# Optimization experiments

Hardware: AMD Instinct MI355X
Metric: run time of the kernel (lower is better)

The kernel has to match this reference:

```python
import jax, jax.numpy as jnp
import numpy as np

B, T, N, CIN = 64, 24, 256, 1  # batch, n_his, n stations, in channels
F1, F2, OUTC = 64, 128, 1      # blocks [[64,64],[64,128]], output channels
K = 3                          # conv kernel size


def conv2d_same(x, w):  # x [B,H,W,C], w [K,K,C,O]
    return jax.lax.conv_general_dilated(x, w, (1, 1), 'SAME',
                                        dimension_numbers=('NHWC', 'HWIO', 'NHWC'))


def conv1d_same(x, w):  # x [B,N,C], w [K,C,O]
    return jax.lax.conv_general_dilated(x, w, (1,), 'SAME',
                                        dimension_numbers=('NWC', 'WIO', 'NWC'))


def hard_sigmoid(x):  # keras ConvLSTM default recurrent_activation
    return jnp.clip(x * 0.2 + 0.5, 0.0, 1.0)


def l2_normalize_23(x):  # tf.nn.l2_normalize over axes [2,3]
    sq = jnp.sum(x * x, axis=(2, 3), keepdims=True)
    return x * jax.lax.rsqrt(jnp.maximum(sq, 1e-12))


def convlstm1d(x_seq, kx, kh, b, return_sequences):
    # x_seq [B,T,N,C]; kx [K,C,4F]; kh [K,F,4F]; b [4F]
    Bs, Ts, Ns, Cs = x_seq.shape
    F = kh.shape[1]
    # input convolutions are time-independent: do them all at once
    xg = conv1d_same(x_seq.reshape(Bs * Ts, Ns, Cs), kx).reshape(Bs, Ts, Ns, 4 * F) + b
    xg = jnp.moveaxis(xg, 1, 0)  # [T,B,N,4F]
    h0 = jnp.zeros((Bs, Ns, F), x_seq.dtype)
    c0 = jnp.zeros((Bs, Ns, F), x_seq.dtype)

    def step(carry, xt):
        h, c = carry
        g = xt + conv1d_same(h, kh)                 # [B,N,4F]
        gi, gf, gc, go = jnp.split(g, 4, axis=-1)
        i = hard_sigmoid(gi)
        f = hard_sigmoid(gf)
        o = hard_sigmoid(go)
        c = f * c + i * jnp.tanh(gc)
        h = o * jnp.tanh(c)
        return (h, c), (h if return_sequences else jnp.zeros((), x_seq.dtype))

    (hT, _), hs = jax.lax.scan(step, (h0, c0), xg)
    if return_sequences:
        return jnp.moveaxis(hs, 0, 1)  # [B,T,N,F]
    return hT                          # [B,N,F]


def setup_inputs() -> dict:
    key = jax.random.key(0)
    ks = jax.random.split(key, 14)
    s = 0.1
    return {
        'x': jax.random.normal(ks[0], (B, T, N, CIN), jnp.float32),
        'conv1_w': jax.random.normal(ks[1], (K, K, CIN, F1), jnp.float32) * s,
        'conv1_b': jnp.zeros((F1,), jnp.float32),
        'conv2_w': jax.random.normal(ks[2], (K, K, F1, F1), jnp.float32) * s,
        'conv2_b': jnp.zeros((F1,), jnp.float32),
        'kx1': jax.random.normal(ks[3], (K, F1, 4 * F1), jnp.float32) * s,
        'kh1': jax.random.normal(ks[4], (K, F1, 4 * F1), jnp.float32) * s,
        'b1': jnp.zeros((4 * F1,), jnp.float32),
        'kx2': jax.random.normal(ks[5], (K, F1, 4 * F2), jnp.float32) * s,
        'kh2': jax.random.normal(ks[6], (K, F2, 4 * F2), jnp.float32) * s,
        'b2': jnp.zeros((4 * F2,), jnp.float32),
        'fc_w': jax.random.normal(ks[7], (F2, OUTC), jnp.float32) * s,
        'fc_b': jnp.zeros((OUTC,), jnp.float32),
    }


def reference(x, conv1_w, conv1_b, conv2_w, conv2_b, kx1, kh1, b1,
              kx2, kh2, b2, fc_w, fc_b):
    # spatial conv stack (Conv2D 3x3 same, linear activation)
    h = conv2d_same(x, conv1_w) + conv1_b
    h = conv2d_same(h, conv2_w) + conv2_b
    # dropout = identity at inference; norm == 'L2'
    h = l2_normalize_23(h)
    # stacked ConvLSTM1D: return_sequences=True then False
    h = convlstm1d(h, kx1, kh1, b1, True)    # [B,T,N,F1]
    h = convlstm1d(h, kx2, kh2, b2, False)   # [B,N,F2]
    h = h[:, None]                            # reshape (-1, 1, N, F2)
    h = l2_normalize_23(h)
    # FullyConLayer: 1x1 FC over channels -> outc
    y = jnp.einsum('bunc,co->buno', h, fc_w) + fc_b
    return y.reshape(-1, 1, N, OUTC)
```

## Files before the change

kernel.cpp:

```cpp
#include <hip/hip_runtime.h>
#include <hip/hip_bf16.h>

using bf16 = __hip_bfloat16;
typedef unsigned short u16;
typedef unsigned int u32;
typedef __attribute__((ext_vector_type(8))) short short8;
typedef __attribute__((ext_vector_type(4))) float floatx4;

#define DEVI __device__ __forceinline__

constexpr int B = 64, T = 24, N = 256, F1 = 64, F2 = 128;

DEVI float b2f(bf16 v) { return __bfloat162float(v); }
DEVI float b2fu(u16 u) { return __uint_as_float(((u32)u) << 16); }
DEVI u16 f2b(float f) {
    u32 u = __float_as_uint(f);
    u32 r = (u + 0x7FFF + ((u >> 16) & 1)) >> 16;
    return (u16)r;
}
DEVI float hsig(float x) { x = x * 0.2f + 0.5f; return fminf(fmaxf(x, 0.f), 1.f); }

#if __has_builtin(__builtin_amdgcn_global_load_lds)
#define ASYNC16(gsrc, ldst)                                                            \
    __builtin_amdgcn_global_load_lds((const __attribute__((address_space(1))) u32*)(gsrc), \
                                     (__attribute__((address_space(3))) u32*)(ldst), 16, 0, 0)
#define HAVE_ASYNC 1
#else
#define HAVE_ASYNC 0
#endif

DEVI float read_in(const void* p, long i, int isbf) {
    return isbf ? b2f(((const bf16*)p)[i]) : ((const float*)p)[i];
}

__global__ void init_flag(int* flag) { *flag = 1; }
__global__ void detect_scan(const u16* __restrict__ xu, int* __restrict__ flag) {
    int i0 = blockIdx.x * 2048 + threadIdx.x;
    int hit = 0;
    for (int i = i0; i < (blockIdx.x + 1) * 2048; i += 256)
        if (((xu[i] >> 7) & 0xFF) == 0xFF) hit = 1;
    if (hit) *flag = 0;
}

struct CvtDesc { const void* src; float* dst; int n; };
struct CvtPack { CvtDesc d[8]; };
__global__ void cvt_pack(CvtPack p, const int* __restrict__ flag) {
    CvtDesc c = p.d[blockIdx.x];
    int isbf = *flag;
    for (int i = threadIdx.x; i < c.n; i += 256)
        c.dst[i] = c.src ? read_in(c.src, i, isbf) : 0.f;
}

__global__ void repack_w(const void* __restrict__ kxr, const void* __restrict__ khr,
                         u16* __restrict__ Wt, int CIN, int F, const int* __restrict__ flag) {
    int NG = 4 * F, CH = CIN + F, K = 3 * CH;
    int idx = blockIdx.x * 256 + threadIdx.x;
    if (idx >= NG * K) return;
    int g = idx / K, k = idx - g * K;
    int kn = k / CH, c = k - kn * CH;
    int isbf = *flag;
    float v = (c < CIN) ? read_in(kxr, (long)(kn * CIN + c) * NG + g, isbf)
                        : read_in(khr, (long)(kn * F + (c - CIN)) * NG + g, isbf);
    Wt[(long)g * K + k] = f2b(v);
}

__global__ void repack_w2(const void* __restrict__ w2r, u16* __restrict__ w2b,
                          const int* __restrict__ flag) {
    int idx = blockIdx.x * 256 + threadIdx.x;
    if (idx >= 64 * 576) return;
    int f = idx / 576, k = idx - f * 576;
    int kt = k / 192, rem = k - kt * 192, kn = rem >> 6, c = rem & 63;
    float v = read_in(w2r, (long)((kt * 3 + kn) * 64 + c) * 64 + f, *flag);
    w2b[(long)f * 576 + k] = f2b(v);
}

__global__ __launch_bounds__(256)
void conv1_all(const void* __restrict__ xraw, const float* __restrict__ w1c,
               const float* __restrict__ b1v, u16* __restrict__ c1all,
               const int* __restrict__ flag) {
    __shared__ float sxw[3 * 260];
    int s = blockIdx.x, b = blockIdx.y, tid = threadIdx.x;
    int tt = s - 1;
    u16* dst = c1all + ((long)s * B + b) * N * 64;
    if (tt < 0 || tt >= T) {
        for (int i = tid; i < N * 64 / 4; i += 256) *(uint2*)&dst[i * 4] = uint2{0, 0};
        return;
    }
    int isbf = *flag;
    for (int i = tid; i < 3 * 258; i += 256) {
        int r = i / 258, cc = i - r * 258;
        int ttt = tt - 1 + r, nn = cc - 1;
        float v = 0.f;
        if (ttt >= 0 && ttt < T && nn >= 0 && nn < N)
            v = read_in(xraw, (long)(b * T + ttt) * N + nn, isbf);
        sxw[r * 260 + cc] = v;
    }
    __syncthreads();
    int c = tid & 63, ngq = tid >> 6;
    float w[9];
#pragma unroll
    for (int j = 0; j < 9; j++) w[j] = w1c[j * 64 + c];
    float bias = b1v[c];
    for (int j = 0; j < 64; j++) {
        int n = ngq * 64 + j;
        float v = bias;
#pragma unroll
        for (int dt = 0; dt < 3; dt++)
#pragma unroll
            for (int dn = 0; dn < 3; dn++)
                v += sxw[dt * 260 + n + dn] * w[dt * 3 + dn];
        dst[n * 64 + c] = f2b(v);
    }
}

__global__ __launch_bounds__(256)
void conv_mfma(const u16* __restrict__ c1all, const u16* __restrict__ w2b,
               const float* __restrict__ b2v, u16* __restrict__ xs24,
               float* __restrict__ ssq) {
    constexpr int CP1 = 72;
    __shared__ __align__(16) u16 win1[3 * 66 * CP1];
    __shared__ __align__(16) u16 bch[2 * 2048];
    __shared__ float red[256];

    int tid = threadIdx.x;
    int bb = blockIdx.y, n0 = blockIdx.x * 64, t = blockIdx.z;
    int w = tid >> 6, l15 = tid & 15, q = (tid >> 4) & 3;

    for (int i = tid; i < 3 * 66 * 8; i += 256) {
        int u = i & 7, rr = i >> 3;
        int kt = rr / 66, r1 = rr - kt * 66;
        int nn = n0 - 1 + r1;
        uint4 v{0, 0, 0, 0};
        if (nn >= 0 && nn < N)
            v = *(const uint4*)&c1all[((((long)(t + kt)) * B + bb) * N + nn) * 64 + u * 8];
        *(uint4*)&win1[(kt * 66 + r1) * CP1 + u * 8] = v;
    }

    auto stage = [&](int kk, int bufi) {
        int g = tid >> 2, u = tid & 3;
        int k = kk * 32 + ((u ^ (g & 3)) << 3);
#if HAVE_ASYNC
        ASYNC16(w2b + (long)g * 576 + k, &bch[bufi * 2048 + tid * 8]);
#else
        uint4 v = *(const uint4*)(w2b + (long)g * 576 + k);
        *(uint4*)&bch[bufi * 2048 + tid * 8] = v;
#endif
    };
    stage(0, 0);
    __syncthreads();

    floatx4 acc[4] = {};
    for (int kk = 0; kk < 18; ++kk) {
        int cur = kk & 1;
        if (kk + 1 < 18) stage(kk + 1, 1 - cur);
        int kbase = kk * 32;
        int kt = kbase / 192, rem = kbase - kt * 192, kn = rem >> 6, c0 = rem & 63;
        int gcol = w * 16 + l15;
        short8 bf = *(const short8*)&bch[cur * 2048 + gcol * 32 + ((q ^ (gcol & 3)) << 3)];
#pragma unroll
        for (int mi = 0; mi < 4; mi++) {
            short8 af = *(const short8*)&win1[(kt * 66 + mi * 16 + l15 + kn) * CP1 + c0 + q * 8];
            acc[mi] = __builtin_amdgcn_mfma_f32_16x16x32_bf16(af, bf, acc[mi], 0, 0, 0);
        }
        __syncthreads();
    }

    u16* xslice = xs24 + (long)t * B * N * 64;
    int f = w * 16 + l15;
    float bias2 = b2v[f];
    float lsum = 0.f;
#pragma unroll
    for (int mi = 0; mi < 4; mi++)
#pragma unroll
        for (int r = 0; r < 4; r++) {
            int n = n0 + mi * 16 + q * 4 + r;
            float v = acc[mi][r] + bias2;
            lsum += v * v;
            xslice[((long)bb * N + n) * 64 + f] = f2b(v);
        }
    red[tid] = lsum; __syncthreads();
    for (int k = 128; k > 0; k >>= 1) {
        if (tid < k) red[tid] += red[tid + k];
        __syncthreads();
    }
    if (tid == 0) atomicAdd(&ssq[bb * T + t], red[0]);
}

__global__ __launch_bounds__(512, 2)
void lstm1_chain(const u16* __restrict__ xs24, u16* __restrict__ h1all,
                 const u16* __restrict__ Wt, const float* __restrict__ bias,
                 const float* __restrict__ ssq) {
    constexpr int CHP = 136;
    constexpr int NGP = 260;
    __shared__ __align__(16) u16 win[114 * CHP];
    __shared__ __align__(16) float Gld[112 * NGP];

    int tid = threadIdx.x;
    int bb = blockIdx.y, n0 = blockIdx.x * 64;
    int lo = n0 - 23; if (lo < 0) lo = 0;
    int w = tid >> 6, l15 = tid & 15, q = (tid >> 4) & 3;

    uint4 breg[2][12];
#pragma unroll
    for (int ni = 0; ni < 2; ni++) {
        int g = (2 * w + ni) * 16 + l15;
#pragma unroll
        for (int kk = 0; kk < 12; kk++)
            breg[ni][kk] = *(const uint4*)&Wt[(long)g * 384 + kk * 32 + q * 8];
    }

    float bi[2], bf_[2], bc[2], bo[2];
    (void)bi; (void)bf_; (void)bc; (void)bo;

    for (int i = tid; i < 114 * CHP / 4; i += 512) *(uint2*)&win[i * 4] = uint2{0, 0};
    __syncthreads();

    auto stage_x = [&](int t) {
        float scale = rsqrtf(fmaxf(ssq[bb * T + t], 1e-12f));
        const u16* xsl = xs24 + (long)t * B * N * 64;
        for (int i = tid; i < 114 * 16; i += 512) {
            int r = i >> 4, gi = i & 15;
            int n = lo - 1 + r;
            uint2 v{};
            if (n >= 0 && n < N) {
                v = *(const uint2*)&xsl[((long)bb * N + n) * 64 + gi * 4];
                u16 e0 = f2b(b2fu((u16)(v.x & 0xFFFF)) * scale);
                u16 e1 = f2b(b2fu((u16)(v.x >> 16)) * scale);
                u16 e2 = f2b(b2fu((u16)(v.y & 0xFFFF)) * scale);
                u16 e3 = f2b(b2fu((u16)(v.y >> 16)) * scale);
                v.x = (u32)e0 | ((u32)e1 << 16);
                v.y = (u32)e2 | ((u32)e3 << 16);
            }
            *(uint2*)&win[r * CHP + gi * 4] = v;
        }
    };
    stage_x(0);
    __syncthreads();

    float cst[14];
#pragma unroll
    for (int j = 0; j < 14; j++) cst[j] = 0.f;

    for (int t = 0; t < T; ++t) {
        floatx4 acc[7][2] = {};
        for (int kk = 0; kk < 12; ++kk) {
            int kn = kk >> 2, c0 = (kk & 3) * 32;
#pragma unroll
            for (int mi = 0; mi < 7; mi++) {
                short8 af = *(const short8*)&win[(mi * 16 + l15 + kn) * CHP + c0 + q * 8];
#pragma unroll
                for (int ni = 0; ni < 2; ni++)
                    acc[mi][ni] = __builtin_amdgcn_mfma_f32_16x16x32_bf16(
                        af, *(short8*)&breg[ni][kk], acc[mi][ni], 0, 0, 0);
            }
        }
#pragma unroll
        for (int mi = 0; mi < 7; mi++)
#pragma unroll
            for (int ni = 0; ni < 2; ni++) {
                int g = (2 * w + ni) * 16 + l15;
#pragma unroll
                for (int r = 0; r < 4; r++)
                    Gld[(mi * 16 + q * 4 + r) * NGP + g] = acc[mi][ni][r];
            }
        __syncthreads();

#pragma unroll
        for (int j = 0; j < 14; j++) {
            int p = tid + j * 512;
            int m = p >> 6, f = p & 63;
            float gi = Gld[m * NGP + f]        + bias[f];
            float gf = Gld[m * NGP + 64 + f]   + bias[64 + f];
            float gc = Gld[m * NGP + 128 + f]  + bias[128 + f];
            float go = Gld[m * NGP + 192 + f]  + bias[192 + f];
            float iv = hsig(gi), fv = hsig(gf), ov = hsig(go);
            float cn = fv * cst[j] + iv * tanhf(gc);
            cst[j] = cn;
            int n = lo + m;
            if (n < N) {
                u16 hb = f2b(ov * tanhf(cn));
                win[(m + 1) * CHP + 64 + f] = hb;
                if ((unsigned)(n - n0) < 64u)
                    h1all[((long)t * B + bb) * N * 64 + n * 64 + f] = hb;
            }
        }
        if (t + 1 < T) stage_x(t + 1);
        __syncthreads();
    }
}

template<int CIN, int F, int FL>
__global__ __launch_bounds__(512, 4)
void lstm_mfma(const u16* __restrict__ xin, const u16* __restrict__ hprev,
               u16* __restrict__ hnext, float* __restrict__ cst,
               const u16* __restrict__ Wt, const float* __restrict__ bias,
               const float* __restrict__ ssqp, int t) {
    constexpr int CH = CIN + F;
    constexpr int CHP = CH + 8;
    constexpr int K = 3 * CH;
    constexpr int NK = K / 32;
    constexpr int NGL = 4 * FL;
    constexpr int NGP = NGL + 4;
    constexpr int NI = NGL / 128;
    constexpr int BCH = NGL * 32;
    constexpr int GLD_USH = 32 * NGP * 2;
    constexpr int UNION_USH = (2 * BCH > GLD_USH) ? 2 * BCH : GLD_USH;
    constexpr int LOGFL = (FL == 64) ? 6 : 5;

    __shared__ __align__(16) u16 win[66 * CHP];
    __shared__ __align__(16) u16 ubuf[UNION_USH];
    u16* bch = ubuf;
    float* Gld = (float*)ubuf;

    int tid = threadIdx.x;
    int bb = blockIdx.y, n0 = blockIdx.x * 64, z = blockIdx.z;
    int w = tid >> 6, l15 = tid & 15, q = (tid >> 4) & 3;

    float scale = 1.f;
    if (ssqp) scale = rsqrtf(fmaxf(ssqp[bb * T + t], 1e-12f));

    constexpr int GRP = CH / 4;
    for (int i = tid; i < 66 * GRP; i += 512) {
        int row = i / GRP, g4 = (i - row * GRP) * 4;
        int n = n0 + row - 1;
        uint2 v{};
        if (n >= 0 && n < N) {
            if (g4 < CIN) {
                v = *(const uint2*)&xin[((long)bb * N + n) * CIN + g4];
                if (ssqp) {
                    u16 e0 = f2b(b2fu((u16)(v.x & 0xFFFF)) * scale);
                    u16 e1 = f2b(b2fu((u16)(v.x >> 16)) * scale);
                    u16 e2 = f2b(b2fu((u16)(v.y & 0xFFFF)) * scale);
                    u16 e3 = f2b(b2fu((u16)(v.y >> 16)) * scale);
                    v.x = (u32)e0 | ((u32)e1 << 16);
                    v.y = (u32)e2 | ((u32)e3 << 16);
                }
            } else if (t > 0) {
                v = *(const uint2*)&hprev[((long)bb * N + n) * F + (g4 - CIN)];
            }
        }
        *(uint2*)&win[row * CHP + g4] = v;
    }

    auto stage = [&](int kk, int bufi) {
#pragma unroll
        for (int it = 0; it < NGL / 128; ++it) {
            int P = it * 512 + tid;
            int r = P >> 2, u = P & 3;
            int gt = r >> LOGFL, fl = r & (FL - 1);
            long g = (long)gt * F + z * FL + fl;
            int k = kk * 32 + ((u ^ (r & 3)) << 3);
#if HAVE_ASYNC
            ASYNC16(Wt + g * K + k, &bch[bufi * BCH + P * 8]);
#else
            uint4 v = *(const uint4*)(Wt + g * K + k);
            *(uint4*)&bch[bufi * BCH + P * 8] = v;
#endif
        }
    };
    stage(0, 0);
    __syncthreads();

    floatx4 acc[4][NI] = {};
    for (int kk = 0; kk < NK; ++kk) {
        int cur = kk & 1;
        if (kk + 1 < NK) stage(kk + 1, 1 - cur);
        int kbase = kk * 32;
        int kn = kbase / CH, c0 = kbase - kn * CH;
        short8 af[4];
#pragma unroll
        for (int mi = 0; mi < 4; mi++)
            af[mi] = *(const short8*)&win[(mi * 16 + l15 + kn) * CHP + c0 + q * 8];
#pragma unroll
        for (int ni = 0; ni < NI; ni++) {
            int r = w * (NI * 16) + ni * 16 + l15;
            short8 bf = *(const short8*)&bch[cur * BCH + r * 32 + ((q ^ (r & 3)) << 3)];
#pragma unroll
            for (int mi = 0; mi < 4; mi++)
                acc[mi][ni] = __builtin_amdgcn_mfma_f32_16x16x32_bf16(af[mi], bf, acc[mi][ni], 0, 0, 0);
        }
        __syncthreads();
    }

    for (int h = 0; h < 2; ++h) {
#pragma unroll
        for (int mi2 = 0; mi2 < 2; ++mi2) {
            int mi = h * 2 + mi2;
#pragma unroll
            for (int ni = 0; ni < NI; ni++)
#pragma unroll
                for (int r = 0; r < 4; r++)
                    Gld[(mi2 * 16 + q * 4 + r) * NGP + w * (NI * 16) + ni * 16 + l15] = acc[mi][ni][r];
        }
        __syncthreads();
        for (int i = tid; i < 32 * FL; i += 512) {
            int m = i >> LOGFL, fl = i & (FL - 1);
            int fz = z * FL + fl;
            float gi = Gld[m * NGP + fl]          + bias[fz];
            float gf = Gld[m * NGP + FL + fl]     + bias[F + fz];
            float gc = Gld[m * NGP + 2 * FL + fl] + bias[2 * F + fz];
            float go = Gld[m * NGP + 3 * FL + fl] + bias[3 * F + fz];
            int n = n0 + h * 32 + m;
            long ci = ((long)bb * N + n) * F + fz;
            float cp = (t > 0) ? cst[ci] : 0.f;
            float iv = hsig(gi), fv = hsig(gf), ov = hsig(go);
            float cn = fv * cp + iv * tanhf(gc);
            cst[ci] = cn;
            hnext[ci] = f2b(ov * tanhf(cn));
        }
        __syncthreads();
    }
}

__global__ void final_kernel(const u16* __restrict__ hT, const float* __restrict__ fcw,
                             const float* __restrict__ fcb, void* __restrict__ out,
                             const int* __restrict__ flag) {
    __shared__ float red[256];
    int b = blockIdx.x, tid = threadIdx.x;
    const u16* hb = hT + (long)b * N * 128;
    float s = 0.f;
    for (int i = tid; i < N * 128; i += 256) { float v = b2fu(hb[i]); s += v * v; }
    red[tid] = s; __syncthreads();
    for (int k = 128; k > 0; k >>= 1) {
        if (tid < k) red[tid] += red[tid + k];
        __syncthreads();
    }
    float scale = rsqrtf(fmaxf(red[0], 1e-12f));
    int n = tid;
    float acc = fcb[0];
    for (int c = 0; c < 128; c++) acc += b2fu(hb[n * 128 + c]) * scale * fcw[c];
    if (*flag) ((bf16*)out)[b * N + n] = __float2bfloat16(acc);
    else       ((float*)out)[b * N + n] = acc;
}

extern "C" void kernel_launch(void* const* d_in, const int* in_sizes, int n_in,
                              void* d_out, int out_size, void* d_ws, size_t ws_size,
                              hipStream_t stream) {
    float* ws = (float*)d_ws;
    u16* xs24   = (u16*)ws;
    u16* c1all  = (u16*)(ws + 12582912);
    u16* h1all  = (u16*)(ws + 26214400);
    u16* h2A    = (u16*)(ws + 38797312);
    u16* h2B    = (u16*)(ws + 39845888);
    float* c2   = ws + 40894464;
    u16* Wt1    = (u16*)(ws + 42991616);
    u16* Wt2    = (u16*)(ws + 43040768);
    u16* w2b    = (u16*)(ws + 43188224);
    float* w1c  = ws + 43206656;
    float* bb1  = ws + 43207232;
    float* bb2  = ws + 43207296;
    float* bg1  = ws + 43207360;
    float* bg2  = ws + 43207616;
    float* fcwf = ws + 43208128;
    float* fcbf = ws + 43208256;
    float* ssq  = ws + 43208257;
    int*   flag = (int*)(ws + 43209793);

    init_flag<<<1, 1, 0, stream>>>(flag);
    detect_scan<<<32, 256, 0, stream>>>((const u16*)d_in[0], flag);

    CvtPack pk;
    pk.d[0] = {d_in[1],  w1c,  576};
    pk.d[1] = {d_in[2],  bb1,  64};
    pk.d[2] = {d_in[4],  bb2,  64};
    pk.d[3] = {d_in[7],  bg1,  256};
    pk.d[4] = {d_in[10], bg2,  512};
    pk.d[5] = {d_in[11], fcwf, 128};
    pk.d[6] = {d_in[12], fcbf, 1};
    pk.d[7] = {nullptr,  ssq,  B * T};
    cvt_pack<<<8, 256, 0, stream>>>(pk, flag);

    repack_w<<<(256 * 384 + 255) / 256, 256, 0, stream>>>(d_in[5], d_in[6], Wt1, 64, 64, flag);
    repack_w<<<(512 * 576 + 255) / 256, 256, 0, stream>>>(d_in[8], d_in[9], Wt2, 64, 128, flag);
    repack_w2<<<(64 * 576 + 255) / 256, 256, 0, stream>>>(d_in[3], w2b, flag);

    conv1_all<<<dim3(26, B), 256, 0, stream>>>(d_in[0], w1c, bb1, c1all, flag);
    conv_mfma<<<dim3(4, B, 24), 256, 0, stream>>>(c1all, w2b, bb2, xs24, ssq);

    lstm1_chain<<<dim3(4, B), 512, 0, stream>>>(xs24, h1all, Wt1, bg1, ssq);

    for (int t = 0; t < T; t++) {
        const u16* h2p = (t & 1) ? h2A : h2B;
        u16* h2n = (t & 1) ? h2B : h2A;
        lstm_mfma<64, 128, 64><<<dim3(4, B, 2), 512, 0, stream>>>(
            h1all + (long)t * B * N * 64, h2p, h2n, c2, Wt2, bg2, nullptr, t);
    }
    final_kernel<<<B, 256, 0, stream>>>(h2B, fcwf, fcbf, d_out, flag);
}
```

Baseline: 879.2 us.

## Chunk second ConvLSTM over 8 timesteps per launch with halo recompute

Replaces the 24 per-timestep launches of the second ConvLSTM layer with 3 launches, each running 8 timesteps inside one block. Each block keeps hidden and cell state in shared memory over an 80-row window with an 8-row halo, so neighbouring blocks need no exchange between steps. Gate weights are interleaved per feature (i,f,c,o adjacent), which lets the gate combination happen in registers through lane shuffles instead of a shared-memory round trip. The cost is redundant halo computation (80 rows computed for 64 kept), all 4F gates per block instead of splitting over z, larger shared-memory use and lower occupancy.

```diff
diff --git a/kernel.cpp b/kernel.cpp
--- a/kernel.cpp
+++ b/kernel.cpp
@@ -62,6 +62,20 @@
     float v = (c < CIN) ? read_in(kxr, (long)(kn * CIN + c) * NG + g, isbf)
                         : read_in(khr, (long)(kn * F + (c - CIN)) * NG + g, isbf);
     Wt[(long)g * K + k] = f2b(v);
+}
+
+__global__ void repack_w2i(const void* __restrict__ kxr, const void* __restrict__ khr,
+                           u16* __restrict__ Wt, const int* __restrict__ flag) {
+    int idx = blockIdx.x * 256 + threadIdx.x;
+    if (idx >= 512 * 576) return;
+    int gp = idx / 576, k = idx - gp * 576;
+    int f = gp >> 2, gate = gp & 3;
+    int srccol = gate * 128 + f;
+    int kn = k / 192, c = k - kn * 192;
+    int isbf = *flag;
+    float v = (c < 64) ? read_in(kxr, (long)(kn * 64 + c) * 512 + srccol, isbf)
+                       : read_in(khr, (long)(kn * 128 + (c - 64)) * 512 + srccol, isbf);
+    Wt[(long)gp * 576 + k] = f2b(v);
 }
 
 __global__ void repack_w2(const void* __restrict__ w2r, u16* __restrict__ w2b,
@@ -208,9 +222,6 @@
         for (int kk = 0; kk < 12; kk++)
             breg[ni][kk] = *(const uint4*)&Wt[(long)g * 384 + kk * 32 + q * 8];
     }
-
-    float bi[2], bf_[2], bc[2], bo[2];
-    (void)bi; (void)bf_; (void)bc; (void)bo;
 
     for (int i = tid; i < 114 * CHP / 4; i += 512) *(uint2*)&win[i * 4] = uint2{0, 0};
     __syncthreads();
@@ -289,125 +300,121 @@
     }
 }
 
-template<int CIN, int F, int FL>
-__global__ __launch_bounds__(512, 4)
-void lstm_mfma(const u16* __restrict__ xin, const u16* __restrict__ hprev,
-               u16* __restrict__ hnext, float* __restrict__ cst,
-               const u16* __restrict__ Wt, const float* __restrict__ bias,
-               const float* __restrict__ ssqp, int t) {
-    constexpr int CH = CIN + F;
-    constexpr int CHP = CH + 8;
-    constexpr int K = 3 * CH;
-    constexpr int NK = K / 32;
-    constexpr int NGL = 4 * FL;
-    constexpr int NGP = NGL + 4;
-    constexpr int NI = NGL / 128;
-    constexpr int BCH = NGL * 32;
-    constexpr int GLD_USH = 32 * NGP * 2;
-    constexpr int UNION_USH = (2 * BCH > GLD_USH) ? 2 * BCH : GLD_USH;
-    constexpr int LOGFL = (FL == 64) ? 6 : 5;
-
-    __shared__ __align__(16) u16 win[66 * CHP];
-    __shared__ __align__(16) u16 ubuf[UNION_USH];
-    u16* bch = ubuf;
-    float* Gld = (float*)ubuf;
+__global__ __launch_bounds__(512, 2)
+void lstm2_chunk(const u16* __restrict__ h1all, u16* __restrict__ h2state,
+                 float* __restrict__ c2state, const u16* __restrict__ Wt,
+                 const float* __restrict__ bias, int t0) {
+    constexpr int CHP2 = 200;
+    constexpr int C2S = 132;
+    __shared__ __align__(16) u16 win[82 * CHP2];
+    __shared__ __align__(16) u16 bch[2 * 16384];
+    __shared__ __align__(16) float c2buf[80 * C2S];
 
     int tid = threadIdx.x;
-    int bb = blockIdx.y, n0 = blockIdx.x * 64, z = blockIdx.z;
+    int bb = blockIdx.y, n0 = blockIdx.x * 64;
+    int lo = n0 - 8; if (lo < 0) lo = 0; if (lo > N - 80) lo = N - 80;
     int w = tid >> 6, l15 = tid & 15, q = (tid >> 4) & 3;
-
-    float scale = 1.f;
-    if (ssqp) scale = rsqrtf(fmaxf(ssqp[bb * T + t], 1e-12f));
-
-    constexpr int GRP = CH / 4;
-    for (int i = tid; i < 66 * GRP; i += 512) {
-        int row = i / GRP, g4 = (i - row * GRP) * 4;
-        int n = n0 + row - 1;
+    bool first = (t0 == 0);
+
+    for (int i = tid; i < 82 * 32; i += 512) {
+        int r = i >> 5, gi = i & 31;
+        int n = lo - 1 + r;
         uint2 v{};
-        if (n >= 0 && n < N) {
-            if (g4 < CIN) {
-                v = *(const uint2*)&xin[((long)bb * N + n) * CIN + g4];
-                if (ssqp) {
-                    u16 e0 = f2b(b2fu((u16)(v.x & 0xFFFF)) * scale);
-                    u16 e1 = f2b(b2fu((u16)(v.x >> 16)) * scale);
-                    u16 e2 = f2b(b2fu((u16)(v.y & 0xFFFF)) * scale);
-                    u16 e3 = f2b(b2fu((u16)(v.y >> 16)) * scale);
-                    v.x = (u32)e0 | ((u32)e1 << 16);
-                    v.y = (u32)e2 | ((u32)e3 << 16);
-                }
-            } else if (t > 0) {
-                v = *(const uint2*)&hprev[((long)bb * N + n) * F + (g4 - CIN)];
-            }
-        }
-        *(uint2*)&win[row * CHP + g4] = v;
-    }
-
-    auto stage = [&](int kk, int bufi) {
-#pragma unroll
-        for (int it = 0; it < NGL / 128; ++it) {
+        if (!first && n >= 0 && n < N)
+            v = *(const uint2*)&h2state[((long)bb * N + n) * 128 + gi * 4];
+        *(uint2*)&win[r * CHP2 + 64 + gi * 4] = v;
+    }
+    for (int i = tid; i < 80 * 32; i += 512) {
+        int m = i >> 5, g4 = (i & 31) * 4;
+        int n = lo + m;
+        float4 v = {0.f, 0.f, 0.f, 0.f};
+        if (!first) v = *(const float4*)&c2state[((long)bb * N + n) * 128 + g4];
+        *(float4*)&c2buf[m * C2S + g4] = v;
+    }
+
+    auto stage_h1 = [&](int t) {
+        const u16* src = h1all + (long)t * B * N * 64;
+        for (int i = tid; i < 82 * 16; i += 512) {
+            int r = i >> 4, gi = i & 15;
+            int n = lo - 1 + r;
+            uint2 v{};
+            if (n >= 0 && n < N) v = *(const uint2*)&src[((long)bb * N + n) * 64 + gi * 4];
+            *(uint2*)&win[r * CHP2 + gi * 4] = v;
+        }
+    };
+    auto stage_b = [&](int kk, int bufi) {
+#pragma unroll
+        for (int it = 0; it < 4; ++it) {
             int P = it * 512 + tid;
             int r = P >> 2, u = P & 3;
-            int gt = r >> LOGFL, fl = r & (FL - 1);
-            long g = (long)gt * F + z * FL + fl;
             int k = kk * 32 + ((u ^ (r & 3)) << 3);
 #if HAVE_ASYNC
-            ASYNC16(Wt + g * K + k, &bch[bufi * BCH + P * 8]);
+            ASYNC16(Wt + (long)r * 576 + k, &bch[bufi * 16384 + P * 8]);
 #else
-            uint4 v = *(const uint4*)(Wt + g * K + k);
-            *(uint4*)&bch[bufi * BCH + P * 8] = v;
+            uint4 v = *(const uint4*)(Wt + (long)r * 576 + k);
+            *(uint4*)&bch[bufi * 16384 + P * 8] = v;
 #endif
         }
     };
-    stage(0, 0);
+    stage_h1(t0);
+    stage_b(0, 0);
     __syncthreads();
 
-    floatx4 acc[4][NI] = {};
-    for (int kk = 0; kk < NK; ++kk) {
-        int cur = kk & 1;
-        if (kk + 1 < NK) stage(kk + 1, 1 - cur);
-        int kbase = kk * 32;
-        int kn = kbase / CH, c0 = kbase - kn * CH;
-        short8 af[4];
-#pragma unroll
-        for (int mi = 0; mi < 4; mi++)
-            af[mi] = *(const short8*)&win[(mi * 16 + l15 + kn) * CHP + c0 + q * 8];
-#pragma unroll
-        for (int ni = 0; ni < NI; ni++) {
-            int r = w * (NI * 16) + ni * 16 + l15;
-            short8 bf = *(const short8*)&bch[cur * BCH + r * 32 + ((q ^ (r & 3)) << 3)];
-#pragma unroll
-            for (int mi = 0; mi < 4; mi++)
-                acc[mi][ni] = __builtin_amdgcn_mfma_f32_16x16x32_bf16(af[mi], bf, acc[mi][ni], 0, 0, 0);
-        }
-        __syncthreads();
-    }
-
-    for (int h = 0; h < 2; ++h) {
-#pragma unroll
-        for (int mi2 = 0; mi2 < 2; ++mi2) {
-            int mi = h * 2 + mi2;
-#pragma unroll
-            for (int ni = 0; ni < NI; ni++)
-#pragma unroll
-                for (int r = 0; r < 4; r++)
-                    Gld[(mi2 * 16 + q * 4 + r) * NGP + w * (NI * 16) + ni * 16 + l15] = acc[mi][ni][r];
-        }
-        __syncthreads();
-        for (int i = tid; i < 32 * FL; i += 512) {
-            int m = i >> LOGFL, fl = i & (FL - 1);
-            int fz = z * FL + fl;
-            float gi = Gld[m * NGP + fl]          + bias[fz];
-            float gf = Gld[m * NGP + FL + fl]     + bias[F + fz];
-            float gc = Gld[m * NGP + 2 * FL + fl] + bias[2 * F + fz];
-            float go = Gld[m * NGP + 3 * FL + fl] + bias[3 * F + fz];
-            int n = n0 + h * 32 + m;
-            long ci = ((long)bb * N + n) * F + fz;
-            float cp = (t > 0) ? cst[ci] : 0.f;
-            float iv = hsig(gi), fv = hsig(gf), ov = hsig(go);
-            float cn = fv * cp + iv * tanhf(gc);
-            cst[ci] = cn;
-            hnext[ci] = f2b(ov * tanhf(cn));
-        }
+    for (int t = t0; t < t0 + 8; ++t) {
+        floatx4 acc[5][4] = {};
+        for (int kk = 0; kk < 18; ++kk) {
+            int cur = kk & 1;
+            if (kk + 1 < 18) stage_b(kk + 1, 1 - cur);
+            int kbase = kk * 32;
+            int kn = kbase / 192, c0 = kbase - kn * 192;
+            short8 af[5];
+#pragma unroll
+            for (int mi = 0; mi < 5; mi++)
+                af[mi] = *(const short8*)&win[(mi * 16 + l15 + kn) * CHP2 + c0 + q * 8];
+#pragma unroll
+            for (int ni = 0; ni < 4; ni++) {
+                int r = w * 64 + ni * 16 + l15;
+                short8 bf = *(const short8*)&bch[cur * 16384 + r * 32 + ((q ^ (r & 3)) << 3)];
+#pragma unroll
+                for (int mi = 0; mi < 5; mi++)
+                    acc[mi][ni] = __builtin_amdgcn_mfma_f32_16x16x32_bf16(af[mi], bf, acc[mi][ni], 0, 0, 0);
+            }
+            __syncthreads();
+        }
+        bool last = (t == t0 + 7);
+        bool act = (l15 & 3) == 0;
+        int fo = l15 >> 2;
+#pragma unroll
+        for (int mi = 0; mi < 5; mi++)
+#pragma unroll
+            for (int ni = 0; ni < 4; ni++)
+#pragma unroll
+                for (int r = 0; r < 4; r++) {
+                    float v = acc[mi][ni][r];
+                    float v1 = __shfl_xor(v, 1);
+                    float v2 = __shfl_xor(v, 2);
+                    float v3 = __shfl_xor(v, 3);
+                    if (act) {
+                        int m = mi * 16 + q * 4 + r;
+                        int ff = w * 16 + ni * 4 + fo;
+                        float gi = v  + bias[ff];
+                        float gf = v1 + bias[128 + ff];
+                        float gc = v2 + bias[256 + ff];
+                        float go = v3 + bias[384 + ff];
+                        float cp = c2buf[m * C2S + ff];
+                        float iv = hsig(gi), fv = hsig(gf), ov = hsig(go);
+                        float cn = fv * cp + iv * tanhf(gc);
+                        c2buf[m * C2S + ff] = cn;
+                        u16 hb = f2b(ov * tanhf(cn));
+                        win[(m + 1) * CHP2 + 64 + ff] = hb;
+                        int n = lo + m;
+                        if (last && (unsigned)(n - n0) < 64u) {
+                            h2state[((long)bb * N + n) * 128 + ff] = hb;
+                            c2state[((long)bb * N + n) * 128 + ff] = cn;
+                        }
+                    }
+                }
+        if (!last) { stage_h1(t + 1); stage_b(0, 0); }
         __syncthreads();
     }
 }
@@ -437,24 +444,23 @@
                               void* d_out, int out_size, void* d_ws, size_t ws_size,
                               hipStream_t stream) {
     float* ws = (float*)d_ws;
-    u16* xs24   = (u16*)ws;
-    u16* c1all  = (u16*)(ws + 12582912);
-    u16* h1all  = (u16*)(ws + 26214400);
-    u16* h2A    = (u16*)(ws + 38797312);
-    u16* h2B    = (u16*)(ws + 39845888);
-    float* c2   = ws + 40894464;
-    u16* Wt1    = (u16*)(ws + 42991616);
-    u16* Wt2    = (u16*)(ws + 43040768);
-    u16* w2b    = (u16*)(ws + 43188224);
-    float* w1c  = ws + 43206656;
-    float* bb1  = ws + 43207232;
-    float* bb2  = ws + 43207296;
-    float* bg1  = ws + 43207360;
-    float* bg2  = ws + 43207616;
-    float* fcwf = ws + 43208128;
-    float* fcbf = ws + 43208256;
-    float* ssq  = ws + 43208257;
-    int*   flag = (int*)(ws + 43209793);
+    u16* xs24    = (u16*)ws;
+    u16* c1all   = (u16*)(ws + 12582912);
+    u16* h1all   = (u16*)(ws + 26214400);
+    u16* h2state = (u16*)(ws + 38797312);
+    float* c2state = ws + 39845888;
+    u16* Wt1     = (u16*)(ws + 41943040);
+    u16* Wt2i    = (u16*)(ws + 41992192);
+    u16* w2b     = (u16*)(ws + 42139648);
+    float* w1c   = ws + 42158080;
+    float* bb1   = ws + 42158656;
+    float* bb2   = ws + 42158720;
+    float* bg1   = ws + 42158784;
+    float* bg2   = ws + 42159040;
+    float* fcwf  = ws + 42159552;
+    float* fcbf  = ws + 42159680;
+    float* ssq   = ws + 42159681;
+    int*   flag  = (int*)(ws + 42161217);
 
     init_flag<<<1, 1, 0, stream>>>(flag);
     detect_scan<<<32, 256, 0, stream>>>((const u16*)d_in[0], flag);
@@ -471,7 +477,7 @@
     cvt_pack<<<8, 256, 0, stream>>>(pk, flag);
 
     repack_w<<<(256 * 384 + 255) / 256, 256, 0, stream>>>(d_in[5], d_in[6], Wt1, 64, 64, flag);
-    repack_w<<<(512 * 576 + 255) / 256, 256, 0, stream>>>(d_in[8], d_in[9], Wt2, 64, 128, flag);
+    repack_w2i<<<(512 * 576 + 255) / 256, 256, 0, stream>>>(d_in[8], d_in[9], Wt2i, flag);
     repack_w2<<<(64 * 576 + 255) / 256, 256, 0, stream>>>(d_in[3], w2b, flag);
 
     conv1_all<<<dim3(26, B), 256, 0, stream>>>(d_in[0], w1c, bb1, c1all, flag);
@@ -479,11 +485,8 @@
 
     lstm1_chain<<<dim3(4, B), 512, 0, stream>>>(xs24, h1all, Wt1, bg1, ssq);
 
-    for (int t = 0; t < T; t++) {
-        const u16* h2p = (t & 1) ? h2A : h2B;
-        u16* h2n = (t & 1) ? h2B : h2A;
-        lstm_mfma<64, 128, 64><<<dim3(4, B, 2), 512, 0, stream>>>(
-            h1all + (long)t * B * N * 64, h2p, h2n, c2, Wt2, bg2, nullptr, t);
-    }
-    final_kernel<<<B, 256, 0, stream>>>(h2B, fcwf, fcbf, d_out, flag);
-}
+    for (int c = 0; c < 3; c++)
+        lstm2_chunk<<<dim3(4, B), 512, 0, stream>>>(h1all, h2state, c2state, Wt2i, bg2, c * 8);
+
+    final_kernel<<<B, 256, 0, stream>>>(h2state, fcwf, fcbf, d_out, flag);
+}
```

Measured after the change: 1.710 ms. 1.95x slower.
